# Performance work log

Measured on AMD Instinct MI355X. Metric: run time of the kernel, lower is better.

The kernel has to match this reference:

```python
import jax, jax.numpy as jnp
import numpy as np
from jax import lax

B, D_IN, H, D_OUT, DEPTH = 16384, 1024, 1024, 256, 7


def setup_inputs() -> dict:
    key = jax.random.key(0)
    ks = jax.random.split(key, 10)
    f = jax.random.normal
    return {
        "x": f(ks[0], (B, D_IN), dtype=jnp.float32),
        "w0": f(ks[1], (D_IN, H), dtype=jnp.float32),
        "b0": f(ks[2], (H,), dtype=jnp.float32),
        "w1": f(ks[3], (H, H), dtype=jnp.float32),
        "b1": f(ks[4], (H,), dtype=jnp.float32),
        "tw": f(ks[5], (DEPTH, H, H), dtype=jnp.float32),   # transcendent_weights
        "cw": f(ks[6], (H, H), dtype=jnp.float32),           # classical_weights
        "cb": f(ks[7], (H,), dtype=jnp.float32),             # classical_biases (+ transcendent_biases folded out; original never uses transcendent_biases in forward)
        "wout": f(ks[8], (H, D_OUT), dtype=jnp.float32),
        "bout": f(ks[9], (D_OUT,), dtype=jnp.float32),
    }


def _transcendent_probs(tw):
    # tw: (DEPTH, n, m); angles used are tw[depth, j, 0:3] for j in range(out_dim)
    D, n, _ = tw.shape
    out_dim = n  # square layer: output_dimensions == input_dimensions
    angles = tw[:, :out_dim, :3]  # (D, O, 3)
    # each 'gate' matrix is the circulant M[i,i]=cos, M[i,i+1]=-sin, M[i+1,i]=sin (indices mod n)
    # => (M s)[i] = cos*s[i] - sin*s[i+1] + sin*s[i-1]  (circular shifts)
    state0 = jnp.full((out_dim, n), 1.0 / np.sqrt(n), dtype=tw.dtype)

    def gate(st, ang):  # st: (O, n), ang: (O,)
        c = jnp.cos(ang)[:, None]
        s = jnp.sin(ang)[:, None]
        return c * st - s * jnp.roll(st, -1, axis=1) + s * jnp.roll(st, 1, axis=1)

    def depth_step(st, a3):  # a3: (O, 3) -> consciousness, intelligence, wisdom gates
        st = gate(st, a3[:, 0])
        st = gate(st, a3[:, 1])
        st = gate(st, a3[:, 2])
        return st, None

    state, _ = lax.scan(depth_step, state0, angles)
    return jnp.abs(state[:, 0]) ** 2  # (O,), identical for every batch row


def reference(x, w0, b0, w1, b1, tw, cw, cb, wout, bout):
    h = jax.nn.relu(x @ w0 + b0)
    h = jax.nn.relu(h @ w1 + b1)
    # TranscendentNeuralLayer: tanh(classical + transcendent)
    h = jnp.tanh(h @ cw + cb + _transcendent_probs(tw)[None, :])
    return jax.nn.relu(h @ wout + bout)
```

## Files before the change

### kernel.cpp

```cpp
#include <hip/hip_runtime.h>
#include <hip/hip_bf16.h>

typedef __attribute__((ext_vector_type(8))) short bf16x8;
typedef __attribute__((ext_vector_type(4))) float f32x4;
typedef __attribute__((ext_vector_type(16))) float f32x16;
typedef unsigned short u16;

__device__ __forceinline__ u16 f2bf(float f) {
  union { float f; unsigned int u; } v; v.f = f;
  unsigned int r = v.u + 0x7fffu + ((v.u >> 16) & 1u);
  return (u16)(r >> 16);
}
__device__ __forceinline__ float bf2f(u16 h) {
  union { unsigned int u; float f; } v; v.u = ((unsigned int)h) << 16;
  return v.f;
}

__device__ __forceinline__ void gload16(const void* g, void* l) {
  __builtin_amdgcn_global_load_lds(
      (const __attribute__((address_space(1))) unsigned int*)g,
      (__attribute__((address_space(3))) unsigned int*)l, 16, 0, 0);
}

__device__ __forceinline__ void do_transpose(const float* __restrict__ src,
                                             u16* __restrict__ dhi, u16* __restrict__ dlo,
                                             int R, int C, int bx, int by, int tid) {
  __shared__ float t[32][33];
  int c0 = bx * 32, r0 = by * 32;
  int tx = tid & 31, ty = tid >> 5;
  #pragma unroll
  for (int p = 0; p < 4; ++p)
    t[ty + p * 8][tx] = src[(size_t)(r0 + ty + p * 8) * C + c0 + tx];
  __syncthreads();
  #pragma unroll
  for (int p = 0; p < 4; ++p) {
    float v = t[tx][ty + p * 8];
    u16 hi = f2bf(v);
    u16 lo = f2bf(v - bf2f(hi));
    size_t idx = (size_t)(c0 + ty + p * 8) * R + r0 + tx;
    dhi[idx] = hi; dlo[idx] = lo;
  }
}

__global__ void prep_kernel(const float* __restrict__ tw, float* __restrict__ probs,
                            const float* __restrict__ w0, u16* w0hi, u16* w0lo,
                            const float* __restrict__ w1, u16* w1hi, u16* w1lo,
                            const float* __restrict__ cw, u16* cwhi, u16* cwlo,
                            const float* __restrict__ wo, u16* wohi, u16* wolo,
                            const float* __restrict__ x, u16* xhi, u16* xlo) {
  const int b = blockIdx.x, tid = threadIdx.x;
  if (b < 4) {
    int i = b * 256 + tid;
    float p = 1.f;
    for (int d = 0; d < 7; ++d) {
      const float* a = tw + ((size_t)d * 1024 + i) * 1024;
      p *= cosf(a[0]) * cosf(a[1]) * cosf(a[2]);
    }
    probs[i] = p * p * (1.0f / 1024.0f);
  } else if (b < 1028) {
    int bb = b - 4;    do_transpose(w0, w0hi, w0lo, 1024, 1024, bb & 31, bb >> 5, tid);
  } else if (b < 2052) {
    int bb = b - 1028; do_transpose(w1, w1hi, w1lo, 1024, 1024, bb & 31, bb >> 5, tid);
  } else if (b < 3076) {
    int bb = b - 2052; do_transpose(cw, cwhi, cwlo, 1024, 1024, bb & 31, bb >> 5, tid);
  } else if (b < 3332) {
    int bb = b - 3076; do_transpose(wo, wohi, wolo, 1024, 256, bb & 7, bb >> 3, tid);
  } else {
    int i = (b - 3332) * 256 + tid;
    if (i < 16384 * 1024 / 4) {
      float4 v = ((const float4*)x)[i];
      ushort4 h, l;
      h.x = f2bf(v.x); l.x = f2bf(v.x - bf2f(h.x));
      h.y = f2bf(v.y); l.y = f2bf(v.y - bf2f(h.y));
      h.z = f2bf(v.z); l.z = f2bf(v.z - bf2f(h.z));
      h.w = f2bf(v.w); l.w = f2bf(v.w - bf2f(h.w));
      ((ushort4*)xhi)[i] = h; ((ushort4*)xlo)[i] = l;
    }
  }
}

template <int EPI>
__global__ __launch_bounds__(512, 2) void gemm256(
    const u16* __restrict__ Ahi, const u16* __restrict__ Alo,
    const u16* __restrict__ Bhi, const u16* __restrict__ Blo,
    const float* __restrict__ bias, const float* __restrict__ extra,
    u16* __restrict__ Ohi, u16* __restrict__ Olo,
    int N, int K, int nbx) {
  extern __shared__ __align__(16) char smem[];
  const int tid = threadIdx.x;
  const int wave = tid >> 6, lane = tid & 63;

  const int bq = gridDim.x >> 3;
  const int wg = (blockIdx.x & 7) * bq + (blockIdx.x >> 3);
  const int m0 = (wg / nbx) * 256, n0 = (wg % nbx) * 256;

  const int wm = (wave >> 2) * 128;
  const int wn = (wave & 3) * 64;
  const int lr = lane & 31;
  const int kg = lane >> 5;

  f32x16 acc[4][2] = {};
  const int NT = K >> 5;

  auto stage = [&](const u16* __restrict__ G, int gr0, int kt, int ubase) {
    #pragma unroll
    for (int p = 0; p < 2; ++p) {
      const int ch = p * 8 + wave;
      const int off = ch * 1024 + lane * 16;
      const int r = off >> 6;
      const int s = ((off >> 4) & 3) ^ ((r >> 1) & 3);
      const u16* src = G + (size_t)(gr0 + r) * K + kt * 32 + s * 8;
      gload16((const void*)src, (void*)(smem + ubase + ch * 1024));
    }
  };
  auto frag = [&](int ubase, int row, int ks) -> bf16x8 {
    const int s = ks * 2 + kg;
    const int byte = ubase + row * 64 + ((s ^ ((row >> 1) & 3)) << 4);
    return *(const bf16x8*)(smem + byte);
  };

  stage(Ahi, m0, 0, 0);
  stage(Bhi, n0, 0, 32768);
  stage(Alo, m0, 0, 16384);
  stage(Blo, n0, 0, 49152);
  asm volatile("s_waitcnt vmcnt(4)" ::: "memory");
  __builtin_amdgcn_s_barrier();

  for (int kt = 0; kt < NT; ++kt) {
    const int cb = (kt & 1) << 16;
    const int nb = cb ^ 65536;
    const int kn = (kt + 1 == NT) ? 0 : kt + 1;
    bf16x8 ah[4][2], bh[2][2], al[4][2], bl[2][2];

    stage(Ahi, m0, kn, nb);
    stage(Bhi, n0, kn, nb + 32768);
    #pragma unroll
    for (int m = 0; m < 4; ++m)
      #pragma unroll
      for (int ks = 0; ks < 2; ++ks) ah[m][ks] = frag(cb, wm + m * 32 + lr, ks);
    #pragma unroll
    for (int n = 0; n < 2; ++n)
      #pragma unroll
      for (int ks = 0; ks < 2; ++ks) bh[n][ks] = frag(cb + 32768, wn + n * 32 + lr, ks);
    asm volatile("" ::: "memory");
    __builtin_amdgcn_s_barrier();
    __builtin_amdgcn_s_setprio(1);
    #pragma unroll
    for (int m = 0; m < 4; ++m)
      #pragma unroll
      for (int n = 0; n < 2; ++n)
        #pragma unroll
        for (int ks = 0; ks < 2; ++ks)
          acc[m][n] = __builtin_amdgcn_mfma_f32_32x32x16_bf16(ah[m][ks], bh[n][ks], acc[m][n], 0, 0, 0);
    __builtin_amdgcn_s_setprio(0);
    asm volatile("s_waitcnt vmcnt(4)" ::: "memory");
    __builtin_amdgcn_s_barrier();

    stage(Alo, m0, kn, nb + 16384);
    stage(Blo, n0, kn, nb + 49152);
    #pragma unroll
    for (int m = 0; m < 4; ++m)
      #pragma unroll
      for (int ks = 0; ks < 2; ++ks) al[m][ks] = frag(cb + 16384, wm + m * 32 + lr, ks);
    #pragma unroll
    for (int n = 0; n < 2; ++n)
      #pragma unroll
      for (int ks = 0; ks < 2; ++ks) bl[n][ks] = frag(cb + 49152, wn + n * 32 + lr, ks);
    asm volatile("" ::: "memory");
    __builtin_amdgcn_s_barrier();
    __builtin_amdgcn_s_setprio(1);
    #pragma unroll
    for (int m = 0; m < 4; ++m)
      #pragma unroll
      for (int n = 0; n < 2; ++n)
        #pragma unroll
        for (int ks = 0; ks < 2; ++ks) {
          acc[m][n] = __builtin_amdgcn_mfma_f32_32x32x16_bf16(al[m][ks], bh[n][ks], acc[m][n], 0, 0, 0);
          acc[m][n] = __builtin_amdgcn_mfma_f32_32x32x16_bf16(ah[m][ks], bl[n][ks], acc[m][n], 0, 0, 0);
        }
    __builtin_amdgcn_s_setprio(0);
    asm volatile("s_waitcnt vmcnt(4)" ::: "memory");
    __builtin_amdgcn_s_barrier();
  }

  const int ln = lane & 31, lg = lane >> 5;
  float bsum[2];
  #pragma unroll
  for (int n = 0; n < 2; ++n) {
    int col = n0 + wn + n * 32 + ln;
    bsum[n] = bias[col];
    if (EPI == 1) bsum[n] += extra[col];
  }
  #pragma unroll
  for (int m = 0; m < 4; ++m) {
    #pragma unroll
    for (int n = 0; n < 2; ++n) {
      int col = n0 + wn + n * 32 + ln;
      #pragma unroll
      for (int r = 0; r < 16; ++r) {
        int row = m0 + wm + m * 32 + (r & 3) + 8 * (r >> 2) + 4 * lg;
        float v = acc[m][n][r] + bsum[n];
        size_t idx = (size_t)row * N + col;
        if (EPI == 0) {
          v = fmaxf(v, 0.f);
          u16 hi = f2bf(v);
          u16 lo = f2bf(v - bf2f(hi));
          Ohi[idx] = hi; Olo[idx] = lo;
        } else {
          v = 1.f - __fdividef(2.f, __expf(2.f * v) + 1.f);
          Ohi[idx] = f2bf(v);
        }
      }
    }
  }
}

__global__ __launch_bounds__(256, 2) void gemm_l4(
    const u16* __restrict__ A, const u16* __restrict__ B,
    float* __restrict__ P, int M, int N, int K, int kchunk) {
  __shared__ __align__(16) u16 sA[128 * 32];
  __shared__ __align__(16) u16 sB[128 * 32];
  const int tid = threadIdx.x;
  const int wave = tid >> 6, lane = tid & 63;
  const int n0 = blockIdx.x * 128, m0 = blockIdx.y * 128;
  const int koff = blockIdx.z * kchunk;
  const int wm = (wave >> 1) * 64, wn = (wave & 1) * 64;
  f32x4 acc[4][4] = {};
  const int srow = lane >> 2, sslot = (lane & 3) * 8;

  for (int kt = koff; kt < koff + kchunk; kt += 32) {
    #pragma unroll
    for (int j = 0; j < 2; ++j) {
      int c = wave * 2 + j;
      gload16((const void*)(A + (size_t)(m0 + c * 16 + srow) * K + kt + sslot), (void*)&sA[c * 512]);
      gload16((const void*)(B + (size_t)(n0 + c * 16 + srow) * K + kt + sslot), (void*)&sB[c * 512]);
    }
    __syncthreads();
    const int kb = (lane >> 4) * 8;
    bf16x8 bfr[4];
    #pragma unroll
    for (int n = 0; n < 4; ++n)
      bfr[n] = *(const bf16x8*)&sB[(wn + n * 16 + (lane & 15)) * 32 + kb];
    #pragma unroll
    for (int m = 0; m < 4; ++m) {
      bf16x8 a = *(const bf16x8*)&sA[(wm + m * 16 + (lane & 15)) * 32 + kb];
      #pragma unroll
      for (int n = 0; n < 4; ++n)
        acc[m][n] = __builtin_amdgcn_mfma_f32_16x16x32_bf16(a, bfr[n], acc[m][n], 0, 0, 0);
    }
    __syncthreads();
  }

  const int lm = lane >> 4, ln = lane & 15;
  float* Pz = P + (size_t)blockIdx.z * M * N;
  #pragma unroll
  for (int m = 0; m < 4; ++m) {
    int rbase = m0 + wm + m * 16 + lm * 4;
    #pragma unroll
    for (int n = 0; n < 4; ++n) {
      int col = n0 + wn + n * 16 + ln;
      #pragma unroll
      for (int r = 0; r < 4; ++r)
        Pz[(size_t)(rbase + r) * N + col] = acc[m][n][r];
    }
  }
}

__global__ void l4_reduce(const float* __restrict__ P, const float* __restrict__ bias,
                          float* __restrict__ out) {
  int i = blockIdx.x * 256 + threadIdx.x;
  float4 a = ((const float4*)P)[i];
  float4 b = ((const float4*)(P + 16384ull * 256))[i];
  int c0 = (i * 4) & 255;
  float4 o;
  o.x = fmaxf(a.x + b.x + bias[c0 + 0], 0.f);
  o.y = fmaxf(a.y + b.y + bias[c0 + 1], 0.f);
  o.z = fmaxf(a.z + b.z + bias[c0 + 2], 0.f);
  o.w = fmaxf(a.w + b.w + bias[c0 + 3], 0.f);
  ((float4*)out)[i] = o;
}

extern "C" void kernel_launch(void* const* d_in, const int* in_sizes, int n_in,
                              void* d_out, int out_size, void* d_ws, size_t ws_size,
                              hipStream_t stream) {
  const float* x    = (const float*)d_in[0];
  const float* w0   = (const float*)d_in[1];
  const float* b0   = (const float*)d_in[2];
  const float* w1   = (const float*)d_in[3];
  const float* b1   = (const float*)d_in[4];
  const float* tw   = (const float*)d_in[5];
  const float* cw   = (const float*)d_in[6];
  const float* cb   = (const float*)d_in[7];
  const float* wout = (const float*)d_in[8];
  const float* bout = (const float*)d_in[9];
  float* out = (float*)d_out;
  char* ws = (char*)d_ws;
  const size_t MB = 1ull << 20;

  float* probs  = (float*)ws;
  u16* w0Thi = (u16*)(ws + 1 * MB);
  u16* w0Tlo = (u16*)(ws + 3 * MB);
  u16* w1Thi = (u16*)(ws + 5 * MB);
  u16* w1Tlo = (u16*)(ws + 7 * MB);
  u16* cwThi = (u16*)(ws + 9 * MB);
  u16* cwTlo = (u16*)(ws + 11 * MB);
  u16* woThi = (u16*)(ws + 13 * MB);
  u16* woTlo = (u16*)(ws + 13 * MB + 512 * 1024);
  u16* r0hi = (u16*)(ws + 16 * MB);
  u16* r0lo = (u16*)(ws + 48 * MB);
  u16* r1hi = (u16*)(ws + 80 * MB);
  u16* r1lo = (u16*)(ws + 112 * MB);
  float* l4p = (float*)(ws + 16 * MB);

  hipFuncSetAttribute(reinterpret_cast<const void*>(gemm256<0>),
                      hipFuncAttributeMaxDynamicSharedMemorySize, 131072);
  hipFuncSetAttribute(reinterpret_cast<const void*>(gemm256<1>),
                      hipFuncAttributeMaxDynamicSharedMemorySize, 131072);

  prep_kernel<<<19716, 256, 0, stream>>>(tw, probs, w0, w0Thi, w0Tlo,
                                         w1, w1Thi, w1Tlo, cw, cwThi, cwTlo,
                                         wout, woThi, woTlo, x, r0hi, r0lo);

  gemm256<0><<<256, 512, 131072, stream>>>(r0hi, r0lo, w0Thi, w0Tlo, b0, nullptr,
                                           r1hi, r1lo, 1024, 1024, 4);
  gemm256<0><<<256, 512, 131072, stream>>>(r1hi, r1lo, w1Thi, w1Tlo, b1, nullptr,
                                           r0hi, r0lo, 1024, 1024, 4);
  gemm256<1><<<256, 512, 131072, stream>>>(r0hi, r0lo, cwThi, cwTlo, cb, probs,
                                           r1hi, nullptr, 1024, 1024, 4);
  gemm_l4<<<dim3(2, 128, 2), 256, 0, stream>>>(r1hi, woThi, l4p, 16384, 256, 1024, 512);
  l4_reduce<<<4096, 256, 0, stream>>>(l4p, bout, out);
}
```

Measured before the change: 447.4 us.

## Switch split-bf16 GEMM to 16x16x32 MFMA and reorder lo-part staging

The 256x256 split-precision GEMM now uses 16x16x32 bf16 MFMA instructions with 8x4 accumulator tiles instead of 32x32x16 with 4x2 tiles. The fragment layout and epilogue indexing change to match. Blo is now staged together with Ahi/Bhi so the hi*hi and hi*lo products run in the first phase and lo*hi in the second, with the vmcnt waits adjusted. The aim is better MFMA throughput and a better balance of load and compute across the two phases. The cost is more LDS fragment reads per MFMA and more MFMA instructions to issue.

```diff
diff --git a/kernel.cpp b/kernel.cpp
--- a/kernel.cpp
+++ b/kernel.cpp
@@ -3,7 +3,6 @@
 
 typedef __attribute__((ext_vector_type(8))) short bf16x8;
 typedef __attribute__((ext_vector_type(4))) float f32x4;
-typedef __attribute__((ext_vector_type(16))) float f32x16;
 typedef unsigned short u16;
 
 __device__ __forceinline__ u16 f2bf(float f) {
@@ -96,10 +95,9 @@
 
   const int wm = (wave >> 2) * 128;
   const int wn = (wave & 3) * 64;
-  const int lr = lane & 31;
-  const int kg = lane >> 5;
-
-  f32x16 acc[4][2] = {};
+  const int lr = lane & 15, s0 = lane >> 4;
+
+  f32x4 acc[8][4] = {};
   const int NT = K >> 5;
 
   auto stage = [&](const u16* __restrict__ G, int gr0, int kt, int ubase) {
@@ -113,94 +111,82 @@
       gload16((const void*)src, (void*)(smem + ubase + ch * 1024));
     }
   };
-  auto frag = [&](int ubase, int row, int ks) -> bf16x8 {
-    const int s = ks * 2 + kg;
-    const int byte = ubase + row * 64 + ((s ^ ((row >> 1) & 3)) << 4);
+  auto frag = [&](int ubase, int row) -> bf16x8 {
+    const int byte = ubase + row * 64 + ((s0 ^ ((row >> 1) & 3)) << 4);
     return *(const bf16x8*)(smem + byte);
   };
 
   stage(Ahi, m0, 0, 0);
   stage(Bhi, n0, 0, 32768);
+  stage(Blo, n0, 0, 49152);
   stage(Alo, m0, 0, 16384);
-  stage(Blo, n0, 0, 49152);
-  asm volatile("s_waitcnt vmcnt(4)" ::: "memory");
+  asm volatile("s_waitcnt vmcnt(2)" ::: "memory");
   __builtin_amdgcn_s_barrier();
 
   for (int kt = 0; kt < NT; ++kt) {
     const int cb = (kt & 1) << 16;
     const int nb = cb ^ 65536;
     const int kn = (kt + 1 == NT) ? 0 : kt + 1;
-    bf16x8 ah[4][2], bh[2][2], al[4][2], bl[2][2];
+    bf16x8 ah[8], bh[4], bl[4], al[8];
 
     stage(Ahi, m0, kn, nb);
     stage(Bhi, n0, kn, nb + 32768);
-    #pragma unroll
-    for (int m = 0; m < 4; ++m)
-      #pragma unroll
-      for (int ks = 0; ks < 2; ++ks) ah[m][ks] = frag(cb, wm + m * 32 + lr, ks);
-    #pragma unroll
-    for (int n = 0; n < 2; ++n)
-      #pragma unroll
-      for (int ks = 0; ks < 2; ++ks) bh[n][ks] = frag(cb + 32768, wn + n * 32 + lr, ks);
+    stage(Blo, n0, kn, nb + 49152);
+    #pragma unroll
+    for (int m = 0; m < 8; ++m) ah[m] = frag(cb, wm + m * 16 + lr);
+    #pragma unroll
+    for (int n = 0; n < 4; ++n) {
+      bh[n] = frag(cb + 32768, wn + n * 16 + lr);
+      bl[n] = frag(cb + 49152, wn + n * 16 + lr);
+    }
     asm volatile("" ::: "memory");
     __builtin_amdgcn_s_barrier();
     __builtin_amdgcn_s_setprio(1);
     #pragma unroll
-    for (int m = 0; m < 4; ++m)
-      #pragma unroll
-      for (int n = 0; n < 2; ++n)
-        #pragma unroll
-        for (int ks = 0; ks < 2; ++ks)
-          acc[m][n] = __builtin_amdgcn_mfma_f32_32x32x16_bf16(ah[m][ks], bh[n][ks], acc[m][n], 0, 0, 0);
+    for (int m = 0; m < 8; ++m)
+      #pragma unroll
+      for (int n = 0; n < 4; ++n) {
+        acc[m][n] = __builtin_amdgcn_mfma_f32_16x16x32_bf16(ah[m], bh[n], acc[m][n], 0, 0, 0);
+        acc[m][n] = __builtin_amdgcn_mfma_f32_16x16x32_bf16(ah[m], bl[n], acc[m][n], 0, 0, 0);
+      }
     __builtin_amdgcn_s_setprio(0);
-    asm volatile("s_waitcnt vmcnt(4)" ::: "memory");
+    asm volatile("s_waitcnt vmcnt(6)" ::: "memory");
     __builtin_amdgcn_s_barrier();
 
     stage(Alo, m0, kn, nb + 16384);
-    stage(Blo, n0, kn, nb + 49152);
-    #pragma unroll
-    for (int m = 0; m < 4; ++m)
-      #pragma unroll
-      for (int ks = 0; ks < 2; ++ks) al[m][ks] = frag(cb + 16384, wm + m * 32 + lr, ks);
-    #pragma unroll
-    for (int n = 0; n < 2; ++n)
-      #pragma unroll
-      for (int ks = 0; ks < 2; ++ks) bl[n][ks] = frag(cb + 49152, wn + n * 32 + lr, ks);
+    #pragma unroll
+    for (int m = 0; m < 8; ++m) al[m] = frag(cb + 16384, wm + m * 16 + lr);
     asm volatile("" ::: "memory");
     __builtin_amdgcn_s_barrier();
     __builtin_amdgcn_s_setprio(1);
     #pragma unroll
-    for (int m = 0; m < 4; ++m)
-      #pragma unroll
-      for (int n = 0; n < 2; ++n)
-        #pragma unroll
-        for (int ks = 0; ks < 2; ++ks) {
-          acc[m][n] = __builtin_amdgcn_mfma_f32_32x32x16_bf16(al[m][ks], bh[n][ks], acc[m][n], 0, 0, 0);
-          acc[m][n] = __builtin_amdgcn_mfma_f32_32x32x16_bf16(ah[m][ks], bl[n][ks], acc[m][n], 0, 0, 0);
-        }
+    for (int m = 0; m < 8; ++m)
+      #pragma unroll
+      for (int n = 0; n < 4; ++n)
+        acc[m][n] = __builtin_amdgcn_mfma_f32_16x16x32_bf16(al[m], bh[n], acc[m][n], 0, 0, 0);
     __builtin_amdgcn_s_setprio(0);
-    asm volatile("s_waitcnt vmcnt(4)" ::: "memory");
+    asm volatile("s_waitcnt vmcnt(2)" ::: "memory");
     __builtin_amdgcn_s_barrier();
   }
 
-  const int ln = lane & 31, lg = lane >> 5;
-  float bsum[2];
-  #pragma unroll
-  for (int n = 0; n < 2; ++n) {
-    int col = n0 + wn + n * 32 + ln;
+  const int lm = lane >> 4, ln = lane & 15;
+  float bsum[4];
+  #pragma unroll
+  for (int n = 0; n < 4; ++n) {
+    int col = n0 + wn + n * 16 + ln;
     bsum[n] = bias[col];
     if (EPI == 1) bsum[n] += extra[col];
   }
   #pragma unroll
-  for (int m = 0; m < 4; ++m) {
-    #pragma unroll
-    for (int n = 0; n < 2; ++n) {
-      int col = n0 + wn + n * 32 + ln;
-      #pragma unroll
-      for (int r = 0; r < 16; ++r) {
-        int row = m0 + wm + m * 32 + (r & 3) + 8 * (r >> 2) + 4 * lg;
+  for (int m = 0; m < 8; ++m) {
+    int rbase = m0 + wm + m * 16 + lm * 4;
+    #pragma unroll
+    for (int n = 0; n < 4; ++n) {
+      int col = n0 + wn + n * 16 + ln;
+      #pragma unroll
+      for (int r = 0; r < 4; ++r) {
         float v = acc[m][n][r] + bsum[n];
-        size_t idx = (size_t)row * N + col;
+        size_t idx = (size_t)(rbase + r) * N + col;
         if (EPI == 0) {
           v = fmaxf(v, 0.f);
           u16 hi = f2bf(v);
```

After: 427.9 us. 4.4% less time.
